# Kernel tuning notes

Hardware: AMD Instinct MI355X
Metric: run time of the kernel (lower is better)

Reference implementation:

```python
import jax, jax.numpy as jnp
import numpy as np

H = 4096          # hidden_size
NQ = 32           # num query heads
NKV = 8           # num kv heads
D = 128           # head_dim
GRP = NQ // NKV   # query heads per kv head
THETA = 10000.0
SCALE = D ** -0.5


def _rope(x, positions):
    # x: [S, N, D]; neox-style rotate-half over full head_dim
    half = D // 2
    inv_freq = 1.0 / (THETA ** (jnp.arange(0, half, dtype=jnp.float32) / half * 2.0 * 0.5 * 2))
    inv_freq = 1.0 / (THETA ** (jnp.arange(0, D, 2, dtype=jnp.float32) / D))
    freqs = positions.astype(jnp.float32)[:, None] * inv_freq[None, :]  # [S, D/2]
    cos = jnp.cos(freqs)[:, None, :]  # [S,1,D/2]
    sin = jnp.sin(freqs)[:, None, :]
    x1, x2 = x[..., :half], x[..., half:]
    return jnp.concatenate([x1 * cos - x2 * sin, x2 * cos + x1 * sin], axis=-1)


def setup_inputs() -> dict:
    key = jax.random.key(0)
    k1, k2, k3 = jax.random.split(key, 3)
    S = 4096
    return {
        "positions": jnp.arange(S, dtype=jnp.int64 if jax.config.jax_enable_x64 else jnp.int32),
        "hidden_states": jax.random.normal(k1, (S, H), dtype=jnp.float32) * 0.02,
        "w_qkv": jax.random.normal(k2, (H, NQ * D + 2 * NKV * D), dtype=jnp.float32) * 0.02,
        "w_o": jax.random.normal(k3, (NQ * D, H), dtype=jnp.float32) * 0.02,
    }


def reference(positions, hidden_states, w_qkv, w_o):
    S = hidden_states.shape[0]
    qkv = hidden_states @ w_qkv                         # [S, 6144]
    q, k, v = jnp.split(qkv, [NQ * D, NQ * D + NKV * D], axis=-1)
    q = _rope(q.reshape(S, NQ, D), positions)           # [S, NQ, D]
    k = _rope(k.reshape(S, NKV, D), positions)          # [S, NKV, D]
    v = v.reshape(S, NKV, D)
    # GQA: group query heads per kv head
    qg = q.reshape(S, NKV, GRP, D)
    scores = jnp.einsum('sghd,tgd->ghst', qg, k) * SCALE  # [NKV, GRP, S, S]
    causal = positions[:, None] >= positions[None, :]     # [S, S]
    scores = jnp.where(causal[None, None], scores, jnp.finfo(scores.dtype).min)
    probs = jax.nn.softmax(scores, axis=-1)
    attn = jnp.einsum('ghst,tgd->sghd', probs, v).reshape(S, NQ * D)
    return attn @ w_o
```

## Files before the change

### kernel.cpp

```cpp
#include <hip/hip_runtime.h>
#include <hip/hip_bf16.h>
#include <math.h>

#define H_DIM 4096
#define NQ    32
#define NKV   8
#define HD    128
#define GRPQ  4
#define NQKV  6144
#define KOFF  4096
#define VOFF  5120
#define SCALE 0.08838834764831844f

typedef float f32x4 __attribute__((ext_vector_type(4)));
typedef short bf16x8 __attribute__((ext_vector_type(8)));

static __device__ __forceinline__ float bf2f(unsigned short u) {
    return __uint_as_float(((unsigned int)u) << 16);
}
static __device__ __forceinline__ unsigned short f2bf(float f) {
    return __bfloat16_as_ushort(__float2bfloat16(f));
}

static __device__ __forceinline__ void gload_lds16(const void* g, void* l) {
    __builtin_amdgcn_global_load_lds(
        (const __attribute__((address_space(1))) unsigned int*)g,
        (__attribute__((address_space(3))) unsigned int*)l, 16, 0, 0);
}

static __device__ __forceinline__ float4 load4(const float* p) {
    return *reinterpret_cast<const float4*>(p);
}
static __device__ __forceinline__ float4 load4(const unsigned short* p) {
    ushort4 v = *reinterpret_cast<const ushort4*>(p);
    return make_float4(bf2f(v.x), bf2f(v.y), bf2f(v.z), bf2f(v.w));
}

static __device__ __forceinline__ void store1(float* p, float v) { *p = v; }
static __device__ __forceinline__ void store1(unsigned short* p, float v) {
    *p = f2bf(v);
}

#define BM 128
#define BN 128
#define BK 16
#define LPAD 4

template <typename TA, typename TB, typename TC>
__global__ __launch_bounds__(256) void gemm_f32acc(
    const TA* __restrict__ A,
    const TB* __restrict__ B,
    TC* __restrict__ C,
    int M, int N, int K)
{
    __shared__ float As[BK][BM + LPAD];
    __shared__ float Bs[BK][BN + LPAD];

    const int tid = threadIdx.x;
    const int bm  = blockIdx.y * BM;
    const int bn  = blockIdx.x * BN;
    const int tx  = tid & 15;
    const int ty  = tid >> 4;

    float acc[8][8];
#pragma unroll
    for (int i = 0; i < 8; ++i)
#pragma unroll
        for (int j = 0; j < 8; ++j) acc[i][j] = 0.0f;

    for (int k0 = 0; k0 < K; k0 += BK) {
        for (int q = tid; q < (BM * BK) / 4; q += 256) {
            int row = q >> 2;
            int kq  = (q & 3) << 2;
            float4 v = load4(&A[(size_t)(bm + row) * K + k0 + kq]);
            As[kq + 0][row] = v.x;
            As[kq + 1][row] = v.y;
            As[kq + 2][row] = v.z;
            As[kq + 3][row] = v.w;
        }
        for (int q = tid; q < (BK * BN) / 4; q += 256) {
            int k = q >> 5;
            int n = (q & 31) << 2;
            float4 v = load4(&B[(size_t)(k0 + k) * N + bn + n]);
            Bs[k][n + 0] = v.x;
            Bs[k][n + 1] = v.y;
            Bs[k][n + 2] = v.z;
            Bs[k][n + 3] = v.w;
        }
        __syncthreads();

#pragma unroll
        for (int k = 0; k < BK; ++k) {
            float a[8], b[8];
#pragma unroll
            for (int i = 0; i < 8; ++i) a[i] = As[k][ty * 8 + i];
#pragma unroll
            for (int j = 0; j < 8; ++j) b[j] = Bs[k][tx * 8 + j];
#pragma unroll
            for (int i = 0; i < 8; ++i)
#pragma unroll
                for (int j = 0; j < 8; ++j) acc[i][j] += a[i] * b[j];
        }
        __syncthreads();
    }

#pragma unroll
    for (int i = 0; i < 8; ++i) {
        size_t r = (size_t)(bm + ty * 8 + i);
#pragma unroll
        for (int j = 0; j < 8; ++j) {
            int c = bn + tx * 8 + j;
            store1(&C[r * N + c], acc[i][j]);
        }
    }
}

__global__ __launch_bounds__(256) void cvt_f32_bf16(
    const float4* __restrict__ src, ushort4* __restrict__ dst, int n4)
{
    int i = blockIdx.x * 256 + threadIdx.x;
    int stride = gridDim.x * 256;
    for (; i < n4; i += stride) {
        float4 v = src[i];
        dst[i] = make_ushort4(f2bf(v.x), f2bf(v.y), f2bf(v.z), f2bf(v.w));
    }
}

__global__ __launch_bounds__(256) void transpose_f32_bf16(
    const float* __restrict__ src, unsigned short* __restrict__ dst,
    int R, int C)
{
    __shared__ unsigned short tile[32][33];
    const int r0 = blockIdx.y * 32;
    const int c0 = blockIdx.x * 32;
    const int t  = threadIdx.x;
    const int lr  = t >> 3;
    const int lc4 = (t & 7) << 2;

    float4 v = load4(&src[(size_t)(r0 + lr) * C + c0 + lc4]);
    tile[lr][lc4 + 0] = f2bf(v.x);
    tile[lr][lc4 + 1] = f2bf(v.y);
    tile[lr][lc4 + 2] = f2bf(v.z);
    tile[lr][lc4 + 3] = f2bf(v.w);
    __syncthreads();

    ushort4 o = make_ushort4(tile[lc4 + 0][lr], tile[lc4 + 1][lr],
                             tile[lc4 + 2][lr], tile[lc4 + 3][lr]);
    *reinterpret_cast<ushort4*>(&dst[(size_t)(c0 + lr) * R + r0 + lc4]) = o;
}

template <typename TC>
__global__ __launch_bounds__(256) void gemm_bf16_bt(
    const unsigned short* __restrict__ A,
    const unsigned short* __restrict__ BT,
    TC* __restrict__ C,
    int M, int N, int K)
{
    __shared__ unsigned short As[128 * 32];
    __shared__ unsigned short Bs[128 * 32];

    const int tid  = threadIdx.x;
    const int lane = tid & 63;
    const int w    = tid >> 6;
    const int wr   = w >> 1;
    const int wc   = w & 1;
    const int l15  = lane & 15;
    const int l4   = lane >> 4;
    const size_t bm = (size_t)blockIdx.y * 128;
    const size_t bn = (size_t)blockIdx.x * 128;

    f32x4 acc[4][4];
#pragma unroll
    for (int mi = 0; mi < 4; ++mi)
#pragma unroll
        for (int ni = 0; ni < 4; ++ni) acc[mi][ni] = (f32x4){0.f, 0.f, 0.f, 0.f};

    for (int k0 = 0; k0 < K; k0 += 32) {
        __syncthreads();
#pragma unroll
        for (int it = 0; it < 2; ++it) {
            const int cb = (w * 2 + it) * 64;
            const int c  = cb + lane;
            gload_lds16(A  + (bm + (c >> 2)) * K + k0 + (c & 3) * 8,
                        (char*)As + cb * 16);
            gload_lds16(BT + (bn + (c >> 2)) * K + k0 + (c & 3) * 8,
                        (char*)Bs + cb * 16);
        }
        __syncthreads();

        bf16x8 a[4], b[4];
#pragma unroll
        for (int mi = 0; mi < 4; ++mi)
            a[mi] = *reinterpret_cast<const bf16x8*>(
                (char*)As + (wr * 64 + mi * 16 + l15) * 64 + l4 * 16);
#pragma unroll
        for (int ni = 0; ni < 4; ++ni)
            b[ni] = *reinterpret_cast<const bf16x8*>(
                (char*)Bs + (wc * 64 + ni * 16 + l15) * 64 + l4 * 16);
#pragma unroll
        for (int mi = 0; mi < 4; ++mi)
#pragma unroll
            for (int ni = 0; ni < 4; ++ni)
                acc[mi][ni] = __builtin_amdgcn_mfma_f32_16x16x32_bf16(
                    a[mi], b[ni], acc[mi][ni], 0, 0, 0);
    }

#pragma unroll
    for (int mi = 0; mi < 4; ++mi) {
#pragma unroll
        for (int r = 0; r < 4; ++r) {
            size_t row = bm + wr * 64 + mi * 16 + l4 * 4 + r;
#pragma unroll
            for (int ni = 0; ni < 4; ++ni) {
                size_t col = bn + wc * 64 + ni * 16 + l15;
                store1(&C[row * N + col], acc[mi][ni][r]);
            }
        }
    }
}

__global__ __launch_bounds__(256) void rope_kernel(
    unsigned short* __restrict__ qkv,
    const int* __restrict__ pos32,
    int S)
{
    int idx = blockIdx.x * 256 + threadIdx.x;
    int total = S * (NQ + NKV) * (HD / 2);
    if (idx >= total) return;

    int j    = idx & 63;
    int head = (idx >> 6) % (NQ + NKV);
    int s    = idx / (64 * (NQ + NKV));

    const bool is64 = (pos32[1] == 0);
    int pos = is64 ? pos32[2 * s] : pos32[s];

    unsigned short* row = qkv + (size_t)s * NQKV + head * HD;
    float x1 = bf2f(row[j]);
    float x2 = bf2f(row[j + 64]);

    float p = (float)pos;
    float inv_freq = powf(10000.0f, -((float)j) * (1.0f / 64.0f));
    float f = p * inv_freq;
    float sn, cs;
    sincosf(f, &sn, &cs);

    row[j]      = f2bf(x1 * cs - x2 * sn);
    row[j + 64] = f2bf(x2 * cs + x1 * sn);
}

__global__ __launch_bounds__(256, 2) void attn_mfma(
    const unsigned short* __restrict__ qkv,
    unsigned short* __restrict__ attn_out,
    int S)
{
    __shared__ unsigned short Ks[64 * 128];
    __shared__ unsigned short Vts[128 * 64];

    const int tid  = threadIdx.x;
    const int lane = tid & 63;
    const int w    = tid >> 6;
    const int l15  = lane & 15;
    const int l4   = lane >> 4;
    const int h    = blockIdx.y;
    const int g    = h >> 2;
    const int xb   = (int)gridDim.x - 1 - (int)blockIdx.x;
    const int s0   = xb * 128;
    const int qw   = s0 + w * 32;

    bf16x8 qf[2][4];
#pragma unroll
    for (int qt = 0; qt < 2; ++qt) {
        const unsigned short* qrow =
            qkv + (size_t)(qw + qt * 16 + l15) * NQKV + h * HD;
#pragma unroll
        for (int ks = 0; ks < 4; ++ks) {
            bf16x8 v = *reinterpret_cast<const bf16x8*>(qrow + ks * 32 + l4 * 8);
            bf16x8 o;
#pragma unroll
            for (int i = 0; i < 8; ++i)
                o[i] = (short)f2bf(bf2f((unsigned short)v[i]) * SCALE);
            qf[qt][ks] = o;
        }
    }

    f32x4 oacc[2][8];
#pragma unroll
    for (int qt = 0; qt < 2; ++qt)
#pragma unroll
        for (int dt = 0; dt < 8; ++dt) oacc[qt][dt] = (f32x4){0.f, 0.f, 0.f, 0.f};
    float m_r[2] = {-1e30f, -1e30f};
    float l_r[2] = {0.f, 0.f};

    const int nt_max = 2 * xb + 2;
    const int nt_w   = 2 * xb + 1 + (w >> 1);

    for (int t = 0; t < nt_max; ++t) {
        const int t0 = t * 64;
        __syncthreads();

#pragma unroll
        for (int it = 0; it < 4; ++it) {
            const int seg  = it * 4 + w;
            const int clin = seg * 64 + lane;
            const int key  = clin >> 4;
            const int csrc = (clin & 15) ^ (key & 7);
            gload_lds16(qkv + (size_t)(t0 + key) * NQKV + KOFF + g * HD + csrc * 8,
                        (char*)Ks + (size_t)seg * 1024);
        }
#pragma unroll
        for (int it = 0; it < 4; ++it) {
            const int cc  = tid + it * 256;
            const int key = cc & 63;
            const int d0  = (cc >> 6) * 8;
            bf16x8 v = *reinterpret_cast<const bf16x8*>(
                qkv + (size_t)(t0 + key) * NQKV + VOFF + g * HD + d0);
            const int kt   = key >> 4;
            const int slot = 32 * (kt >> 1) + 8 * ((key >> 2) & 3) +
                             4 * (kt & 1) + (key & 3);
#pragma unroll
            for (int j = 0; j < 8; ++j) {
                const int d = d0 + j;
                *reinterpret_cast<unsigned short*>(
                    (char*)Vts + d * 128 + ((((slot >> 3) ^ (d & 7))) << 4) +
                    (slot & 7) * 2) = (unsigned short)v[j];
            }
        }
        __syncthreads();

        if (t >= nt_w) continue;

        f32x4 sacc[4][2];
#pragma unroll
        for (int kt = 0; kt < 4; ++kt) {
            sacc[kt][0] = (f32x4){0.f, 0.f, 0.f, 0.f};
            sacc[kt][1] = (f32x4){0.f, 0.f, 0.f, 0.f};
        }
#pragma unroll
        for (int kt = 0; kt < 4; ++kt) {
            const int key = kt * 16 + l15;
            const char* krow = (const char*)Ks + key * 256;
            const int swz = key & 7;
#pragma unroll
            for (int ks = 0; ks < 4; ++ks) {
                bf16x8 kb = *reinterpret_cast<const bf16x8*>(
                    krow + (((ks * 4 + l4) ^ swz) << 4));
                sacc[kt][0] = __builtin_amdgcn_mfma_f32_16x16x32_bf16(
                    kb, qf[0][ks], sacc[kt][0], 0, 0, 0);
                sacc[kt][1] = __builtin_amdgcn_mfma_f32_16x16x32_bf16(
                    kb, qf[1][ks], sacc[kt][1], 0, 0, 0);
            }
        }

        if (t == nt_w - 1) {
#pragma unroll
            for (int kt = 0; kt < 4; ++kt) {
                const int keyb = t0 + kt * 16 + l4 * 4;
#pragma unroll
                for (int qt = 0; qt < 2; ++qt) {
                    const int qrow = qw + qt * 16 + l15;
#pragma unroll
                    for (int r = 0; r < 4; ++r)
                        if (keyb + r > qrow) sacc[kt][qt][r] = -1e30f;
                }
            }
        }

        float pmax[2];
#pragma unroll
        for (int qt = 0; qt < 2; ++qt) {
            float mx = sacc[0][qt][0];
#pragma unroll
            for (int kt = 0; kt < 4; ++kt)
#pragma unroll
                for (int r = 0; r < 4; ++r) mx = fmaxf(mx, sacc[kt][qt][r]);
            mx = fmaxf(mx, __shfl_xor(mx, 16));
            mx = fmaxf(mx, __shfl_xor(mx, 32));
            pmax[qt] = mx;
        }
        const bool need = (pmax[0] > m_r[0] + 8.f) || (pmax[1] > m_r[1] + 8.f);
        if (__any(need)) {
#pragma unroll
            for (int qt = 0; qt < 2; ++qt) {
                float mnew  = fmaxf(m_r[qt], pmax[qt]);
                float alpha = __expf(m_r[qt] - mnew);
                l_r[qt] *= alpha;
                m_r[qt]  = mnew;
#pragma unroll
                for (int r = 0; r < 4; ++r) {
                    float ar = __shfl(alpha, l4 * 4 + r);
#pragma unroll
                    for (int dt = 0; dt < 8; ++dt) oacc[qt][dt][r] *= ar;
                }
            }
        }

        bf16x8 pa[2][2];
#pragma unroll
        for (int qt = 0; qt < 2; ++qt) {
            float lsum = 0.f;
#pragma unroll
            for (int kt = 0; kt < 4; ++kt) {
#pragma unroll
                for (int r = 0; r < 4; ++r) {
                    float p = __expf(sacc[kt][qt][r] - m_r[qt]);
                    lsum += p;
                    pa[qt][kt >> 1][4 * (kt & 1) + r] = (short)f2bf(p);
                }
            }
            lsum += __shfl_xor(lsum, 16);
            lsum += __shfl_xor(lsum, 32);
            l_r[qt] += lsum;
        }

#pragma unroll
        for (int dt = 0; dt < 8; ++dt) {
            const int d = dt * 16 + l15;
            const char* vrow = (const char*)Vts + d * 128;
            const int swz = d & 7;
#pragma unroll
            for (int ks2 = 0; ks2 < 2; ++ks2) {
                bf16x8 vb = *reinterpret_cast<const bf16x8*>(
                    vrow + (((ks2 * 4 + l4) ^ swz) << 4));
                oacc[0][dt] = __builtin_amdgcn_mfma_f32_16x16x32_bf16(
                    pa[0][ks2], vb, oacc[0][dt], 0, 0, 0);
                oacc[1][dt] = __builtin_amdgcn_mfma_f32_16x16x32_bf16(
                    pa[1][ks2], vb, oacc[1][dt], 0, 0, 0);
            }
        }
    }

#pragma unroll
    for (int qt = 0; qt < 2; ++qt) {
        float linv_own = 1.0f / l_r[qt];
#pragma unroll
        for (int r = 0; r < 4; ++r) {
            float linv = __shfl(linv_own, l4 * 4 + r);
            const int row = qw + qt * 16 + l4 * 4 + r;
            unsigned short* dst = attn_out + (size_t)row * (NQ * HD) + h * HD;
#pragma unroll
            for (int dt = 0; dt < 8; ++dt)
                dst[dt * 16 + l15] = f2bf(oacc[qt][dt][r] * linv);
        }
    }
}

extern "C" void kernel_launch(void* const* d_in, const int* in_sizes, int n_in,
                              void* d_out, int out_size, void* d_ws, size_t ws_size,
                              hipStream_t stream)
{
    const int*   positions = (const int*)d_in[0];
    const float* hidden    = (const float*)d_in[1];
    const float* w_qkv     = (const float*)d_in[2];
    const float* w_o       = (const float*)d_in[3];
    const int S = in_sizes[0];
    const size_t Sz = (size_t)S;

    unsigned short* qkv   = (unsigned short*)d_ws;
    unsigned short* attn  = qkv   + Sz * NQKV;
    unsigned short* hbf   = attn  + Sz * H_DIM;
    unsigned short* wqkvT = hbf   + Sz * H_DIM;
    unsigned short* woT   = wqkvT + (size_t)NQKV * H_DIM;
    const size_t need = (Sz * NQKV + Sz * H_DIM + Sz * H_DIM +
                         (size_t)NQKV * H_DIM + (size_t)H_DIM * H_DIM) *
                        sizeof(unsigned short);

    if (ws_size >= need) {
        int n4 = (S * H_DIM) / 4;
        int cg = (n4 + 255) / 256; if (cg > 2048) cg = 2048;
        cvt_f32_bf16<<<cg, 256, 0, stream>>>(
            (const float4*)hidden, (ushort4*)hbf, n4);
        transpose_f32_bf16<<<dim3(NQKV / 32, H_DIM / 32), 256, 0, stream>>>(
            w_qkv, wqkvT, H_DIM, NQKV);
        transpose_f32_bf16<<<dim3(H_DIM / 32, H_DIM / 32), 256, 0, stream>>>(
            w_o, woT, H_DIM, H_DIM);

        gemm_bf16_bt<unsigned short><<<dim3(NQKV / 128, S / 128), 256, 0, stream>>>(
            hbf, wqkvT, qkv, S, NQKV, H_DIM);

        int total = S * (NQ + NKV) * (HD / 2);
        rope_kernel<<<(total + 255) / 256, 256, 0, stream>>>(qkv, positions, S);

        attn_mfma<<<dim3(S / 128, NQ), 256, 0, stream>>>(qkv, attn, S);

        gemm_bf16_bt<float><<<dim3(H_DIM / 128, S / 128), 256, 0, stream>>>(
            attn, woT, (float*)d_out, S, H_DIM, H_DIM);
    } else {
        gemm_f32acc<float, float, unsigned short>
            <<<dim3(NQKV / BN, S / BM), 256, 0, stream>>>(
                hidden, w_qkv, qkv, S, NQKV, H_DIM);
        int total = S * (NQ + NKV) * (HD / 2);
        rope_kernel<<<(total + 255) / 256, 256, 0, stream>>>(qkv, positions, S);
        attn_mfma<<<dim3(S / 128, NQ), 256, 0, stream>>>(qkv, attn, S);
        gemm_f32acc<unsigned short, float, float>
            <<<dim3(H_DIM / BN, S / BM), 256, 0, stream>>>(
                attn, w_o, (float*)d_out, S, H_DIM, H_DIM);
    }
}
```

Measured before the change: 1.071 ms.

## Double-buffer K/V tiles in attention kernel to overlap loads with MFMA compute

Doubles the LDS buffers for K and V and prefetches the next key tile while the current one is being computed. K goes in through async global-to-LDS loads, and V is held in registers and scattered into the other buffer after compute. This cuts the loop to one barrier per iteration and is meant to hide global-load latency behind the MFMA work. The cost is double the LDS use (64KB per block with launch_bounds 2) and extra VGPRs for the V prefetch, which may lower occupancy.

```diff
diff --git a/kernel.cpp b/kernel.cpp
--- a/kernel.cpp
+++ b/kernel.cpp
@@ -254,8 +254,8 @@
     unsigned short* __restrict__ attn_out,
     int S)
 {
-    __shared__ unsigned short Ks[64 * 128];
-    __shared__ unsigned short Vts[128 * 64];
+    __shared__ unsigned short Ks[2][64 * 128];
+    __shared__ unsigned short Vts[2][128 * 64];
 
     const int tid  = threadIdx.x;
     const int lane = tid & 63;
@@ -295,10 +295,9 @@
     const int nt_max = 2 * xb + 2;
     const int nt_w   = 2 * xb + 1 + (w >> 1);
 
-    for (int t = 0; t < nt_max; ++t) {
-        const int t0 = t * 64;
-        __syncthreads();
-
+    bf16x8 vreg[4];
+
+    auto stage_K = [&](int t0, unsigned short* Kbuf) {
 #pragma unroll
         for (int it = 0; it < 4; ++it) {
             const int seg  = it * 4 + w;
@@ -306,15 +305,25 @@
             const int key  = clin >> 4;
             const int csrc = (clin & 15) ^ (key & 7);
             gload_lds16(qkv + (size_t)(t0 + key) * NQKV + KOFF + g * HD + csrc * 8,
-                        (char*)Ks + (size_t)seg * 1024);
-        }
+                        (char*)Kbuf + (size_t)seg * 1024);
+        }
+    };
+    auto load_V = [&](int t0) {
 #pragma unroll
         for (int it = 0; it < 4; ++it) {
             const int cc  = tid + it * 256;
             const int key = cc & 63;
             const int d0  = (cc >> 6) * 8;
-            bf16x8 v = *reinterpret_cast<const bf16x8*>(
+            vreg[it] = *reinterpret_cast<const bf16x8*>(
                 qkv + (size_t)(t0 + key) * NQKV + VOFF + g * HD + d0);
+        }
+    };
+    auto scatter_V = [&](unsigned short* Vbuf) {
+#pragma unroll
+        for (int it = 0; it < 4; ++it) {
+            const int cc  = tid + it * 256;
+            const int key = cc & 63;
+            const int d0  = (cc >> 6) * 8;
             const int kt   = key >> 4;
             const int slot = 32 * (kt >> 1) + 8 * ((key >> 2) & 3) +
                              4 * (kt & 1) + (key & 3);
@@ -322,112 +331,133 @@
             for (int j = 0; j < 8; ++j) {
                 const int d = d0 + j;
                 *reinterpret_cast<unsigned short*>(
-                    (char*)Vts + d * 128 + ((((slot >> 3) ^ (d & 7))) << 4) +
-                    (slot & 7) * 2) = (unsigned short)v[j];
-            }
-        }
+                    (char*)Vbuf + d * 128 + (((slot >> 3) ^ (d & 7)) << 4) +
+                    (slot & 7) * 2) = (unsigned short)vreg[it][j];
+            }
+        }
+    };
+
+    stage_K(0, Ks[0]);
+    load_V(0);
+    scatter_V(Vts[0]);
+    __syncthreads();
+
+    for (int t = 0; t < nt_max; ++t) {
+        const int cur = t & 1;
+        const bool pre = (t + 1 < nt_max);
+
+        if (pre) {
+            stage_K((t + 1) * 64, Ks[cur ^ 1]);
+            load_V((t + 1) * 64);
+        }
+
+        if (t < nt_w) {
+            const int t0 = t * 64;
+
+            f32x4 sacc[4][2];
+#pragma unroll
+            for (int kt = 0; kt < 4; ++kt) {
+                sacc[kt][0] = (f32x4){0.f, 0.f, 0.f, 0.f};
+                sacc[kt][1] = (f32x4){0.f, 0.f, 0.f, 0.f};
+            }
+#pragma unroll
+            for (int kt = 0; kt < 4; ++kt) {
+                const int key = kt * 16 + l15;
+                const char* krow = (const char*)Ks[cur] + key * 256;
+                const int swz = key & 7;
+#pragma unroll
+                for (int ks = 0; ks < 4; ++ks) {
+                    bf16x8 kb = *reinterpret_cast<const bf16x8*>(
+                        krow + (((ks * 4 + l4) ^ swz) << 4));
+                    sacc[kt][0] = __builtin_amdgcn_mfma_f32_16x16x32_bf16(
+                        kb, qf[0][ks], sacc[kt][0], 0, 0, 0);
+                    sacc[kt][1] = __builtin_amdgcn_mfma_f32_16x16x32_bf16(
+                        kb, qf[1][ks], sacc[kt][1], 0, 0, 0);
+                }
+            }
+
+            if (t == nt_w - 1) {
+#pragma unroll
+                for (int kt = 0; kt < 4; ++kt) {
+                    const int keyb = t0 + kt * 16 + l4 * 4;
+#pragma unroll
+                    for (int qt = 0; qt < 2; ++qt) {
+                        const int qrow = qw + qt * 16 + l15;
+#pragma unroll
+                        for (int r = 0; r < 4; ++r)
+                            if (keyb + r > qrow) sacc[kt][qt][r] = -1e30f;
+                    }
+                }
+            }
+
+            float pmax[2];
+#pragma unroll
+            for (int qt = 0; qt < 2; ++qt) {
+                float mx = sacc[0][qt][0];
+#pragma unroll
+                for (int kt = 0; kt < 4; ++kt)
+#pragma unroll
+                    for (int r = 0; r < 4; ++r) mx = fmaxf(mx, sacc[kt][qt][r]);
+                mx = fmaxf(mx, __shfl_xor(mx, 16));
+                mx = fmaxf(mx, __shfl_xor(mx, 32));
+                pmax[qt] = mx;
+            }
+            const bool need = (pmax[0] > m_r[0] + 8.f) ||
+                              (pmax[1] > m_r[1] + 8.f);
+            if (__any(need)) {
+#pragma unroll
+                for (int qt = 0; qt < 2; ++qt) {
+                    float mnew  = fmaxf(m_r[qt], pmax[qt]);
+                    float alpha = __expf(m_r[qt] - mnew);
+                    l_r[qt] *= alpha;
+                    m_r[qt]  = mnew;
+#pragma unroll
+                    for (int r = 0; r < 4; ++r) {
+                        float ar = __shfl(alpha, l4 * 4 + r);
+#pragma unroll
+                        for (int dt = 0; dt < 8; ++dt) oacc[qt][dt][r] *= ar;
+                    }
+                }
+            }
+
+            bf16x8 pa[2][2];
+#pragma unroll
+            for (int qt = 0; qt < 2; ++qt) {
+                float lsum = 0.f;
+#pragma unroll
+                for (int kt = 0; kt < 4; ++kt) {
+#pragma unroll
+                    for (int r = 0; r < 4; ++r) {
+                        float p = __expf(sacc[kt][qt][r] - m_r[qt]);
+                        lsum += p;
+                        pa[qt][kt >> 1][4 * (kt & 1) + r] = (short)f2bf(p);
+                    }
+                }
+                lsum += __shfl_xor(lsum, 16);
+                lsum += __shfl_xor(lsum, 32);
+                l_r[qt] += lsum;
+            }
+
+#pragma unroll
+            for (int dt = 0; dt < 8; ++dt) {
+                const int d = dt * 16 + l15;
+                const char* vrow = (const char*)Vts[cur] + d * 128;
+                const int swz = d & 7;
+#pragma unroll
+                for (int ks2 = 0; ks2 < 2; ++ks2) {
+                    bf16x8 vb = *reinterpret_cast<const bf16x8*>(
+                        vrow + (((ks2 * 4 + l4) ^ swz) << 4));
+                    oacc[0][dt] = __builtin_amdgcn_mfma_f32_16x16x32_bf16(
+                        pa[0][ks2], vb, oacc[0][dt], 0, 0, 0);
+                    oacc[1][dt] = __builtin_amdgcn_mfma_f32_16x16x32_bf16(
+                        pa[1][ks2], vb, oacc[1][dt], 0, 0, 0);
+                }
+            }
+        }
+
+        if (pre) scatter_V(Vts[cur ^ 1]);
+
         __syncthreads();
-
-        if (t >= nt_w) continue;
-
-        f32x4 sacc[4][2];
-#pragma unroll
-        for (int kt = 0; kt < 4; ++kt) {
-            sacc[kt][0] = (f32x4){0.f, 0.f, 0.f, 0.f};
-            sacc[kt][1] = (f32x4){0.f, 0.f, 0.f, 0.f};
-        }
-#pragma unroll
-        for (int kt = 0; kt < 4; ++kt) {
-            const int key = kt * 16 + l15;
-            const char* krow = (const char*)Ks + key * 256;
-            const int swz = key & 7;
-#pragma unroll
-            for (int ks = 0; ks < 4; ++ks) {
-                bf16x8 kb = *reinterpret_cast<const bf16x8*>(
-                    krow + (((ks * 4 + l4) ^ swz) << 4));
-                sacc[kt][0] = __builtin_amdgcn_mfma_f32_16x16x32_bf16(
-                    kb, qf[0][ks], sacc[kt][0], 0, 0, 0);
-                sacc[kt][1] = __builtin_amdgcn_mfma_f32_16x16x32_bf16(
-                    kb, qf[1][ks], sacc[kt][1], 0, 0, 0);
-            }
-        }
-
-        if (t == nt_w - 1) {
-#pragma unroll
-            for (int kt = 0; kt < 4; ++kt) {
-                const int keyb = t0 + kt * 16 + l4 * 4;
-#pragma unroll
-                for (int qt = 0; qt < 2; ++qt) {
-                    const int qrow = qw + qt * 16 + l15;
-#pragma unroll
-                    for (int r = 0; r < 4; ++r)
-                        if (keyb + r > qrow) sacc[kt][qt][r] = -1e30f;
-                }
-            }
-        }
-
-        float pmax[2];
-#pragma unroll
-        for (int qt = 0; qt < 2; ++qt) {
-            float mx = sacc[0][qt][0];
-#pragma unroll
-            for (int kt = 0; kt < 4; ++kt)
-#pragma unroll
-                for (int r = 0; r < 4; ++r) mx = fmaxf(mx, sacc[kt][qt][r]);
-            mx = fmaxf(mx, __shfl_xor(mx, 16));
-            mx = fmaxf(mx, __shfl_xor(mx, 32));
-            pmax[qt] = mx;
-        }
-        const bool need = (pmax[0] > m_r[0] + 8.f) || (pmax[1] > m_r[1] + 8.f);
-        if (__any(need)) {
-#pragma unroll
-            for (int qt = 0; qt < 2; ++qt) {
-                float mnew  = fmaxf(m_r[qt], pmax[qt]);
-                float alpha = __expf(m_r[qt] - mnew);
-                l_r[qt] *= alpha;
-                m_r[qt]  = mnew;
-#pragma unroll
-                for (int r = 0; r < 4; ++r) {
-                    float ar = __shfl(alpha, l4 * 4 + r);
-#pragma unroll
-                    for (int dt = 0; dt < 8; ++dt) oacc[qt][dt][r] *= ar;
-                }
-            }
-        }
-
-        bf16x8 pa[2][2];
-#pragma unroll
-        for (int qt = 0; qt < 2; ++qt) {
-            float lsum = 0.f;
-#pragma unroll
-            for (int kt = 0; kt < 4; ++kt) {
-#pragma unroll
-                for (int r = 0; r < 4; ++r) {
-                    float p = __expf(sacc[kt][qt][r] - m_r[qt]);
-                    lsum += p;
-                    pa[qt][kt >> 1][4 * (kt & 1) + r] = (short)f2bf(p);
-                }
-            }
-            lsum += __shfl_xor(lsum, 16);
-            lsum += __shfl_xor(lsum, 32);
-            l_r[qt] += lsum;
-        }
-
-#pragma unroll
-        for (int dt = 0; dt < 8; ++dt) {
-            const int d = dt * 16 + l15;
-            const char* vrow = (const char*)Vts + d * 128;
-            const int swz = d & 7;
-#pragma unroll
-            for (int ks2 = 0; ks2 < 2; ++ks2) {
-                bf16x8 vb = *reinterpret_cast<const bf16x8*>(
-                    vrow + (((ks2 * 4 + l4) ^ swz) << 4));
-                oacc[0][dt] = __builtin_amdgcn_mfma_f32_16x16x32_bf16(
-                    pa[0][ks2], vb, oacc[0][dt], 0, 0, 0);
-                oacc[1][dt] = __builtin_amdgcn_mfma_f32_16x16x32_bf16(
-                    pa[1][ks2], vb, oacc[1][dt], 0, 0, 0);
-            }
-        }
     }
 
 #pragma unroll
```

Result: no change. 1.060 ms (-1.0%).
